# Kernel optimization log

Measured on AMD Instinct MI355X. Metric: run time of the kernel, lower is better.

The kernel has to match this reference:

```python
import math
import jax, jax.numpy as jnp
import numpy as np

B, S = 2, 2048
D, H, DK = 1024, 16, 64
M = 16            # nb_features
L = 4             # n_layers
DFF = 4096
VS, VT = 69, 69   # src/tgt vocab
NU = 10000        # num_users
FD = 34           # feature_dim
EPS = 1e-6


def make_pe(seq_len, d_model):
    pos = np.arange(seq_len, dtype=np.float32)[:, None]
    div = np.exp(np.arange(0, d_model, 2, dtype=np.float32) * (-math.log(10000.0) / d_model))
    pe = np.zeros((seq_len, d_model), np.float32)
    pe[:, 0::2] = np.sin(pos * div)
    pe[:, 1::2] = np.cos(pos * div)
    return jnp.asarray(pe)


def gelu_approx(x):
    return 0.5 * x * (1.0 + jnp.tanh(math.sqrt(2.0 / math.pi) * (x + 0.044715 * x ** 3)))


def layer_norm(x, alpha, bias):
    # torch LayerNormalization: unbiased std, eps added to std
    mu = x.mean(-1, keepdims=True)
    var = ((x - mu) ** 2).sum(-1, keepdims=True) / (x.shape[-1] - 1)
    return alpha * (x - mu) / (jnp.sqrt(var) + EPS) + bias


def setup_inputs():
    key = jax.random.key(0)
    ks = jax.random.split(key, 24)
    w = lambda k, shape, s=0.02: (jax.random.normal(k, shape, jnp.float32) * s)
    inp = {}
    inp['ids'] = jax.random.randint(ks[0], (B, S), 0, VS)
    inp['user_ids'] = jax.random.randint(ks[1], (B,), 0, NU)
    inp['id_embed'] = w(ks[2], (VS, D), 1.0)
    inp['feat_proj'] = w(ks[3], (D, FD))
    inp['gamma'] = jnp.float32(1.0)
    inp['gate_logits'] = w(ks[4], (NU, H))
    inp['wq'] = w(ks[5], (L, D, D))
    inp['wk'] = w(ks[6], (L, D, D))
    inp['wv'] = w(ks[7], (L, D, D))
    inp['wo'] = w(ks[8], (L, D, D))
    inp['omega'] = jax.random.normal(ks[9], (L, M, DK), jnp.float32) / math.sqrt(DK)
    inp['ln1_a'] = jnp.ones((L, D)); inp['ln1_b'] = jnp.zeros((L, D))
    inp['ln2_a'] = jnp.ones((L, D)); inp['ln2_b'] = jnp.zeros((L, D))
    inp['ff_w1'] = w(ks[10], (L, DFF, D)); inp['ff_b1'] = jnp.zeros((L, DFF))
    inp['ff_w2'] = w(ks[11], (L, D, DFF)); inp['ff_b2'] = jnp.zeros((L, D))
    inp['fin_a'] = jnp.ones((D,)); inp['fin_b'] = jnp.zeros((D,))
    inp['proj_w'] = w(ks[12], (VT, D)); inp['proj_b'] = jnp.zeros((VT,))
    inp['feat_tbl'] = w(ks[13], (VS, FD), 1.0)
    pm = np.zeros(VS, bool); pm[10:] = True   # ids >= 10 are products
    inp['prod_mask'] = jnp.asarray(pm)
    inp['pe'] = make_pe(S, D)
    return inp


def performer(xn, wq, wk, wv, wo, omega, gate):
    b, sq, _ = xn.shape
    q = (xn @ wq.T).reshape(b, sq, H, DK)
    k = (xn @ wk.T).reshape(b, sq, H, DK)
    v = (xn @ wv.T).reshape(b, sq, H, DK)
    # exp kernel feature map + row normalization
    qp = jnp.exp(-0.5 * (q @ omega.T) ** 2)        # (B,S,H,M)
    kp = jnp.exp(-0.5 * (k @ omega.T) ** 2)
    qp = qp / (qp.sum(-1, keepdims=True) + EPS)
    kp = kp / (kp.sum(-1, keepdims=True) + EPS)
    K_cum = jnp.cumsum(kp, axis=1)                              # (B,S,H,M)
    KV_cum = jnp.cumsum(kp[..., None] * v[..., None, :], axis=1)  # (B,S,H,M,DK)
    # blockwise causal index (block_size_h = block_size_w = 1)
    bh, bw = 1, 1
    ki = jnp.minimum((jnp.arange(sq) // bh + 1) * bw - 1, sq - 1)
    Ks = jnp.take(K_cum, ki, axis=1)
    KVs = jnp.take(KV_cum, ki, axis=1)
    num = jnp.einsum('bshm,bshmd->bshd', qp, KVs)
    den = jnp.sum(qp * Ks, -1, keepdims=True)
    out = num / (den + EPS)
    out = out * gate[:, None, :, None]
    return out.reshape(b, sq, D) @ wo.T


def reference(ids, user_ids, id_embed, feat_proj, gamma, gate_logits,
              wq, wk, wv, wo, omega, ln1_a, ln1_b, ln2_a, ln2_b,
              ff_w1, ff_b1, ff_w2, ff_b2, fin_a, fin_b,
              proj_w, proj_b, feat_tbl, prod_mask, pe):
    # SpecialPlusFeatureLookup
    id_vec = id_embed[ids]                       # (B,S,D)
    feat_vec = feat_tbl[ids] @ feat_proj.T       # (B,S,D)
    keep = prod_mask[ids]
    x = id_vec + gamma * (feat_vec * keep[..., None])
    # positional encoding (dropout=eval -> identity)
    x = x + pe[None, :x.shape[1], :]
    # per-user head gate
    gate = jax.nn.softmax(gate_logits[user_ids], axis=-1)  # (B,H)
    for l in range(L):
        x = x + performer(layer_norm(x, ln1_a[l], ln1_b[l]),
                          wq[l], wk[l], wv[l], wo[l], omega[l], gate)
        xn = layer_norm(x, ln2_a[l], ln2_b[l])
        x = x + (gelu_approx(xn @ ff_w1[l].T + ff_b1[l]) @ ff_w2[l].T + ff_b2[l])
    x = layer_norm(x, fin_a, fin_b)
    return x @ proj_w.T + proj_b                 # (B,S,VT)
```

## Files before the change

kernel.cpp:

```cpp
#include <hip/hip_runtime.h>
#include <hip/hip_bf16.h>
#include <math.h>

constexpr int BB  = 2;
constexpr int SS  = 2048;
constexpr int DD  = 1024;
constexpr int HH  = 16;
constexpr int DKK = 64;
constexpr int MB  = 16;
constexpr int LL  = 4;
constexpr int DF  = 4096;
constexpr int VSZ = 69;
constexpr int VTT = 69;
constexpr int FDD = 34;
constexpr float EPSF = 1e-6f;
constexpr int CL = 32;
constexpr int NC = SS / CL;

typedef unsigned short u16;
typedef unsigned int   u32;
using bf16x8 = __attribute__((ext_vector_type(8))) short;
using f32x4  = __attribute__((ext_vector_type(4))) float;

static __device__ __forceinline__ float b2f(u16 u) {
    union { u32 i; float f; } p; p.i = ((u32)u) << 16; return p.f;
}
static __device__ __forceinline__ u16 f2b(float f) {
    union { float f; u32 i; } p; p.f = f;
    u32 r = p.i + 0x7fffu + ((p.i >> 16) & 1u);
    return (u16)(r >> 16);
}
static __device__ __forceinline__ u32 pack2(float lo, float hi) {
    __hip_bfloat162 h = __float22bfloat162_rn(make_float2(lo, hi));
    return *(u32*)&h;
}
static __device__ __forceinline__ float gelu_f(float x) {
    float z = 0.7978845608028654f * (x + 0.044715f * x * x * x);
    z = fminf(fmaxf(z, -10.f), 10.f);
    float e = __expf(2.f * z);
    float th = (e - 1.f) / (e + 1.f);
    return 0.5f * x * (1.f + th);
}
static __device__ __forceinline__ float ldg1(const void* p, size_t i, int f32) {
    return f32 ? ((const float*)p)[i] : b2f(((const u16*)p)[i]);
}
static __device__ __forceinline__ float4 ldg4(const void* p, size_t i, int f32) {
    if (f32) return *(const float4*)((const float*)p + i);
    ushort4 u = *(const ushort4*)((const u16*)p + i);
    return make_float4(b2f(u.x), b2f(u.y), b2f(u.z), b2f(u.w));
}

#define GLD16(gp, lp) __builtin_amdgcn_global_load_lds( \
    (const __attribute__((address_space(1))) void*)(gp), \
    (__attribute__((address_space(3))) void*)(lp), 16, 0, 0)

__global__ void k_flag(const void* __restrict__ gamma, int* __restrict__ flag) {
    if (threadIdx.x == 0) *flag = (((const u16*)gamma)[0] == 0) ? 1 : 0;
}

__global__ __launch_bounds__(256) void k_build_tbl(
    const void* __restrict__ id_embed, const void* __restrict__ feat_tbl,
    const void* __restrict__ feat_proj, const void* __restrict__ gamma,
    const int* __restrict__ flagp, float* __restrict__ tbl)
{
    const int f32 = *flagp;
    int idx = blockIdx.x * 256 + threadIdx.x;
    if (idx >= VSZ * DD) return;
    int id = idx / DD, d = idx % DD;
    float acc = ldg1(id_embed, idx, f32);
    if (id >= 10) {
        float g = ldg1(gamma, 0, f32);
        float s = 0.f;
        for (int f = 0; f < FDD; ++f)
            s += ldg1(feat_tbl, (size_t)id * FDD + f, f32) * ldg1(feat_proj, (size_t)d * FDD + f, f32);
        acc += g * s;
    }
    tbl[idx] = acc;
}

__global__ __launch_bounds__(256) void k_gather(
    const float* __restrict__ tbl, const int* __restrict__ ids,
    const void* __restrict__ pe, const int* __restrict__ flagp, float* __restrict__ x)
{
    const int f32 = *flagp;
    int idx = blockIdx.x * 256 + threadIdx.x;
    int bs = idx >> 10, d = idx & (DD - 1);
    int s = bs & (SS - 1);
    x[idx] = tbl[ids[bs] * DD + d] + ldg1(pe, (size_t)s * DD + d, f32);
}

__global__ void k_gate(const void* __restrict__ gl, const int* __restrict__ uid,
                       const int* __restrict__ flagp, float* __restrict__ gate)
{
    const int f32 = *flagp;
    int b = threadIdx.x;
    if (b >= BB) return;
    size_t off = (size_t)uid[b] * HH;
    float v[HH], mx = -1e30f;
    for (int i = 0; i < HH; ++i) { v[i] = ldg1(gl, off + i, f32); mx = fmaxf(mx, v[i]); }
    float s = 0.f;
    for (int i = 0; i < HH; ++i) { v[i] = expf(v[i] - mx); s += v[i]; }
    for (int i = 0; i < HH; ++i) gate[b * HH + i] = v[i] / s;
}

__global__ __launch_bounds__(256) void k_layernorm(
    const float* __restrict__ x, const void* __restrict__ alpha,
    const void* __restrict__ beta, size_t p_off,
    const int* __restrict__ flagp, u16* __restrict__ y)
{
    const int f32 = *flagp;
    int row = blockIdx.x;
    const float* xr = x + (size_t)row * DD;
    int t = threadIdx.x;
    float v[4]; float s = 0.f;
    #pragma unroll
    for (int j = 0; j < 4; ++j) { v[j] = xr[t + j * 256]; s += v[j]; }
    __shared__ float red[8];
    int lane = t & 63, wv = t >> 6;
    #pragma unroll
    for (int off = 32; off > 0; off >>= 1) s += __shfl_down(s, off, 64);
    if (lane == 0) red[wv] = s;
    __syncthreads();
    float mu = (red[0] + red[1] + red[2] + red[3]) * (1.f / DD);
    __syncthreads();
    float ss = 0.f;
    #pragma unroll
    for (int j = 0; j < 4; ++j) { float dv = v[j] - mu; ss += dv * dv; }
    #pragma unroll
    for (int off = 32; off > 0; off >>= 1) ss += __shfl_down(ss, off, 64);
    if (lane == 0) red[wv] = ss;
    __syncthreads();
    float var = (red[0] + red[1] + red[2] + red[3]) * (1.f / (DD - 1));
    float rs = 1.f / (sqrtf(var) + EPSF);
    u16* yr = y + (size_t)row * DD;
    #pragma unroll
    for (int j = 0; j < 4; ++j) {
        int d = t + j * 256;
        yr[d] = f2b(ldg1(alpha, p_off + d, f32) * (v[j] - mu) * rs + ldg1(beta, p_off + d, f32));
    }
}

template<int BN, int BK>
static __device__ __forceinline__ void gemm_core(
    const u16* __restrict__ A, int lda,
    const void* __restrict__ W, size_t w_off, int ldw,
    const void* __restrict__ bias, size_t b_off, int f32,
    int K, int O, int act, int mode, u16* __restrict__ Cb, float* __restrict__ resid,
    int bx, int by)
{
    constexpr int NP  = BK / 32;
    constexpr int NI  = (BN == 128) ? 4 : 2;
    constexpr int WCOLS = (BN == 128) ? 4 : 2;
    __shared__ u16 As[NP * 64 * 32];
    __shared__ u16 Bs[NP * BN * 32];
    int t = threadIdx.x;
    int lane = t & 63, w = t >> 6;
    int quad = lane >> 4, l16 = lane & 15;
    int wm = (w / WCOLS) * (NI * 16);
    int wn = (w % WCOLS) * 32;
    int n0 = by * 64, o0 = bx * BN;

    f32x4 acc[NI][2];
    #pragma unroll
    for (int i = 0; i < NI; ++i)
        #pragma unroll
        for (int j = 0; j < 2; ++j)
            #pragma unroll
            for (int r = 0; r < 4; ++r) acc[i][j][r] = 0.f;

    int r0 = t >> 2;
    int swzt = (t >> 3) & 3;
    int c0  = (t & 3) * 8;
    int c0s = ((t & 3) ^ swzt) * 8;
    int tsw = ((t & ~3) | ((t & 3) ^ swzt));
    int quadx = quad ^ ((l16 >> 1) & 3);
    const u16* Ap = A + (size_t)n0 * lda + c0s;
    char* AsB = (char*)As;
    char* BsB = (char*)Bs;

    for (int k0 = 0; k0 < K; k0 += BK) {
        #pragma unroll
        for (int p = 0; p < NP; ++p) {
            int kk = k0 + p * 32;
            char* AsP = AsB + p * 4096;
            char* BsP = BsB + p * (BN * 64);
            GLD16(Ap + (size_t)r0 * lda + kk, AsP + t * 16);
            if (f32) {
                const float* Wf = (const float*)W + w_off + kk + c0;
                const float* q0 = Wf + (size_t)(o0 + r0) * ldw;
                float4 xa = *(const float4*)q0, xb = *(const float4*)(q0 + 4);
                uint4 pk;
                pk.x = pack2(xa.x, xa.y); pk.y = pack2(xa.z, xa.w);
                pk.z = pack2(xb.x, xb.y); pk.w = pack2(xb.z, xb.w);
                *(uint4*)(BsP + tsw * 16) = pk;
                if (BN == 128) {
                    const float* q1 = q0 + (size_t)64 * ldw;
                    float4 ya = *(const float4*)q1, yb = *(const float4*)(q1 + 4);
                    pk.x = pack2(ya.x, ya.y); pk.y = pack2(ya.z, ya.w);
                    pk.z = pack2(yb.x, yb.y); pk.w = pack2(yb.z, yb.w);
                    *(uint4*)(BsP + 4096 + tsw * 16) = pk;
                }
            } else {
                const u16* Wb = (const u16*)W + w_off + kk + c0s;
                GLD16(Wb + (size_t)(o0 + r0) * ldw, BsP + t * 16);
                if (BN == 128)
                    GLD16(Wb + (size_t)(o0 + r0 + 64) * ldw, BsP + 4096 + t * 16);
            }
        }
        __syncthreads();
        #pragma unroll
        for (int p = 0; p < NP; ++p) {
            const u16* AsP = As + p * (64 * 32);
            const u16* BsP = Bs + p * (BN * 32);
            bf16x8 af[NI], bfv[2];
            #pragma unroll
            for (int i = 0; i < NI; ++i)
                af[i] = *(const bf16x8*)(AsP + (size_t)(wm + i * 16 + l16) * 32 + quadx * 8);
            #pragma unroll
            for (int j = 0; j < 2; ++j)
                bfv[j] = *(const bf16x8*)(BsP + (size_t)(wn + j * 16 + l16) * 32 + quadx * 8);
            #pragma unroll
            for (int i = 0; i < NI; ++i)
                #pragma unroll
                for (int j = 0; j < 2; ++j)
                    acc[i][j] = __builtin_amdgcn_mfma_f32_16x16x32_bf16(af[i], bfv[j], acc[i][j], 0, 0, 0);
        }
        __syncthreads();
    }
    #pragma unroll
    for (int i = 0; i < NI; ++i) {
        #pragma unroll
        for (int j = 0; j < 2; ++j) {
            int col = o0 + wn + j * 16 + l16;
            float bval = bias ? ldg1(bias, b_off + col, f32) : 0.f;
            #pragma unroll
            for (int r = 0; r < 4; ++r) {
                int row = n0 + wm + i * 16 + quad * 4 + r;
                float val = acc[i][j][r] + bval;
                if (act) val = gelu_f(val);
                size_t idx = (size_t)row * O + col;
                if (mode == 1)      resid[idx] += val;
                else if (mode == 2) atomicAdd(&resid[idx], val);
                else                Cb[idx] = f2b(val);
            }
        }
    }
}

static __device__ __forceinline__ void xcd_tile(int& bx, int& by) {
    int gx = gridDim.x;
    int nwg = gx * gridDim.y;
    int h = blockIdx.y * gx + blockIdx.x;
    int q = nwg >> 3;
    int lid = (h & 7) * q + (h >> 3);
    bx = lid % gx; by = lid / gx;
}

__global__ __launch_bounds__(256, 8) void k_gemm_a(
    const u16* __restrict__ A, int lda, const void* __restrict__ W, size_t w_off, int ldw,
    const void* __restrict__ bias, size_t b_off, const int* __restrict__ flagp,
    int K, int O, int act, int mode, u16* __restrict__ Cb, float* __restrict__ resid)
{
    int bx, by; xcd_tile(bx, by);
    gemm_core<128, 32>(A, lda, W, w_off, ldw, bias, b_off, *flagp, K, O, act, mode, Cb, resid,
                       bx, by);
}

__global__ __launch_bounds__(256, 8) void k_gemm_b(
    const u16* __restrict__ A, int lda, const void* __restrict__ W, size_t w_off, int ldw,
    const void* __restrict__ bias, size_t b_off, const int* __restrict__ flagp,
    int K, int O, int act, int mode, u16* __restrict__ Cb, float* __restrict__ resid)
{
    int bx, by; xcd_tile(bx, by);
    gemm_core<64, 64>(A, lda, W, w_off, ldw, bias, b_off, *flagp, K, O, act, mode, Cb, resid,
                      bx, by);
}

__global__ __launch_bounds__(256) void k_gemm_qkv(
    const u16* __restrict__ A,
    const void* __restrict__ Wq, const void* __restrict__ Wk, const void* __restrict__ Wv,
    size_t w_off, const int* __restrict__ flagp,
    u16* __restrict__ oq, u16* __restrict__ ok, u16* __restrict__ ov)
{
    const void* W = (blockIdx.z == 0) ? Wq : (blockIdx.z == 1) ? Wk : Wv;
    u16* o = (blockIdx.z == 0) ? oq : (blockIdx.z == 1) ? ok : ov;
    int bx, by; xcd_tile(bx, by);
    gemm_core<128, 64>(A, DD, W, w_off, DD, nullptr, 0, *flagp, DD, DD, 0, 0, o, nullptr,
                       bx, by);
}

__global__ __launch_bounds__(256, 8) void k_gemm_wo(
    const u16* __restrict__ A, const void* __restrict__ W, size_t l_off_w,
    const int* __restrict__ flagp, float* __restrict__ resid)
{
    int c = blockIdx.z;
    int bx, by; xcd_tile(bx, by);
    gemm_core<64, 64>(A + (size_t)c * 512, DD, W, l_off_w + (size_t)c * 512, DD,
                      nullptr, 0, *flagp, 512, DD, 0, 2, nullptr, resid, bx, by);
}

__global__ __launch_bounds__(256, 8) void k_gemm_ff2(
    const u16* __restrict__ A, const void* __restrict__ W, size_t l_off_w,
    const void* __restrict__ bias, size_t l_off_b, const int* __restrict__ flagp,
    float* __restrict__ resid)
{
    int c = blockIdx.z;
    int bx, by; xcd_tile(bx, by);
    gemm_core<64, 64>(A + (size_t)c * 2048, DF, W, l_off_w + (size_t)c * 2048, DF,
                      (c == 0) ? bias : nullptr, l_off_b, *flagp,
                      2048, DD, 0, 2, nullptr, resid, bx, by);
}

__global__ __launch_bounds__(256) void k_gemm_small(
    const u16* __restrict__ A, const void* __restrict__ W, size_t w_off, int ldw,
    const void* __restrict__ bias, size_t b_off,
    const int* __restrict__ flagp, int K, int O, void* __restrict__ outp)
{
    const int f32 = *flagp;
    __shared__ float As[16][68];
    __shared__ float Ws[16][68];
    int t = threadIdx.x;
    int tx = t & 15, ty = t >> 4;
    int o0 = blockIdx.x * 64, n0 = blockIdx.y * 64;
    int lr = t >> 2;
    int lk = (t & 3) * 4;
    float c[4][4] = {};
    for (int k0 = 0; k0 < K; k0 += 16) {
        ushort4 av = *(const ushort4*)(A + (size_t)(n0 + lr) * K + k0 + lk);
        As[lk + 0][lr] = b2f(av.x); As[lk + 1][lr] = b2f(av.y);
        As[lk + 2][lr] = b2f(av.z); As[lk + 3][lr] = b2f(av.w);
        float4 wv4 = make_float4(0.f, 0.f, 0.f, 0.f);
        int orow = o0 + lr;
        if (orow < O) wv4 = ldg4(W, w_off + (size_t)orow * ldw + k0 + lk, f32);
        Ws[lk + 0][lr] = wv4.x; Ws[lk + 1][lr] = wv4.y;
        Ws[lk + 2][lr] = wv4.z; Ws[lk + 3][lr] = wv4.w;
        __syncthreads();
        #pragma unroll
        for (int kk = 0; kk < 16; ++kk) {
            float4 a = *(const float4*)&As[kk][ty * 4];
            float4 b = *(const float4*)&Ws[kk][tx * 4];
            c[0][0] += a.x * b.x; c[0][1] += a.x * b.y; c[0][2] += a.x * b.z; c[0][3] += a.x * b.w;
            c[1][0] += a.y * b.x; c[1][1] += a.y * b.y; c[1][2] += a.y * b.z; c[1][3] += a.y * b.w;
            c[2][0] += a.z * b.x; c[2][1] += a.z * b.y; c[2][2] += a.z * b.z; c[2][3] += a.z * b.w;
            c[3][0] += a.w * b.x; c[3][1] += a.w * b.y; c[3][2] += a.w * b.z; c[3][3] += a.w * b.w;
        }
        __syncthreads();
    }
    #pragma unroll
    for (int i = 0; i < 4; ++i) {
        int n = n0 + ty * 4 + i;
        #pragma unroll
        for (int j = 0; j < 4; ++j) {
            int o = o0 + tx * 4 + j;
            if (o >= O) continue;
            float val = c[i][j];
            if (bias) val += ldg1(bias, b_off + o, f32);
            size_t idx = (size_t)n * O + o;
            if (f32) ((float*)outp)[idx] = val;
            else     ((u16*)outp)[idx] = f2b(val);
        }
    }
}

__global__ __launch_bounds__(256) void k_featmap(
    const u16* __restrict__ q, const void* __restrict__ omega, size_t o_off,
    const int* __restrict__ flagp, u16* __restrict__ qp_t)
{
    const int f32 = *flagp;
    __shared__ float q_s[64][68];
    __shared__ float om_s[16][68];
    int t = threadIdx.x;
    int bh = blockIdx.y, b = bh >> 4, h = bh & 15;
    int s0 = blockIdx.x * 64;
    const u16* qbase = q + (size_t)(b * SS + s0) * DD + h * DKK;
    #pragma unroll
    for (int i = 0; i < 2; ++i) {
        int idx = i * 256 + t;
        int si = idx >> 3, part = idx & 7;
        uint4 raw = *(const uint4*)(qbase + (size_t)si * DD + part * 8);
        const u16* pr = (const u16*)&raw;
        *(float4*)&q_s[si][part * 8]     = make_float4(b2f(pr[0]), b2f(pr[1]), b2f(pr[2]), b2f(pr[3]));
        *(float4*)&q_s[si][part * 8 + 4] = make_float4(b2f(pr[4]), b2f(pr[5]), b2f(pr[6]), b2f(pr[7]));
    }
    #pragma unroll
    for (int i = 0; i < 4; ++i) {
        int idx = i * 256 + t;
        om_s[idx >> 6][idx & 63] = ldg1(omega, o_off + idx, f32);
    }
    __syncthreads();
    int s = t >> 2, mg = t & 3;
    float u[4] = {0.f, 0.f, 0.f, 0.f};
    #pragma unroll
    for (int dk = 0; dk < 64; dk += 4) {
        float4 q4 = *(const float4*)&q_s[s][dk];
        #pragma unroll
        for (int mj = 0; mj < 4; ++mj) {
            float4 o4 = *(const float4*)&om_s[mg * 4 + mj][dk];
            u[mj] += q4.x * o4.x + q4.y * o4.y + q4.z * o4.z + q4.w * o4.w;
        }
    }
    float phi[4], tot = 0.f;
    #pragma unroll
    for (int mj = 0; mj < 4; ++mj) { phi[mj] = expf(-0.5f * u[mj] * u[mj]); tot += phi[mj]; }
    tot += __shfl_xor(tot, 1); tot += __shfl_xor(tot, 2);
    float inv = 1.f / (tot + EPSF);
    uint2 out;
    out.x = pack2(phi[0] * inv, phi[1] * inv);
    out.y = pack2(phi[2] * inv, phi[3] * inv);
    *(uint2*)(qp_t + ((size_t)bh * SS + s0 + s) * MB + mg * 4) = out;
}

__global__ __launch_bounds__(64) void k_scan_part(
    const u16* __restrict__ kp_t, const u16* __restrict__ v,
    float* __restrict__ kv_tot, float* __restrict__ kc_tot)
{
    int c = blockIdx.x, bh = blockIdx.y;
    int b = bh >> 4, h = bh & 15;
    int d = threadIdx.x;
    __shared__ float kp_s[CL * MB];
    const u16* kpb = kp_t + ((size_t)bh * SS + c * CL) * MB;
    #pragma unroll
    for (int i = 0; i < CL * MB / 64; ++i) {
        int idx = i * 64 + d;
        kp_s[idx] = b2f(kpb[idx]);
    }
    __syncthreads();
    float Kc[MB], KV[MB];
    #pragma unroll
    for (int m = 0; m < MB; ++m) { Kc[m] = 0.f; KV[m] = 0.f; }
    const u16* vp = v + ((size_t)b * SS + c * CL) * DD + h * DKK + d;
    for (int si = 0; si < CL; ++si) {
        float vd = b2f(vp[(size_t)si * DD]);
        #pragma unroll
        for (int m = 0; m < MB; ++m) {
            float kp = kp_s[si * MB + m];
            Kc[m] += kp; KV[m] += kp * vd;
        }
    }
    float* kvp = kv_tot + (((size_t)bh * NC + c) * MB) * DKK + d;
    #pragma unroll
    for (int m = 0; m < MB; ++m) kvp[(size_t)m * DKK] = KV[m];
    #pragma unroll
    for (int m = 0; m < MB; ++m)
        if (d == m) kc_tot[((size_t)bh * NC + c) * MB + m] = Kc[m];
}

__global__ __launch_bounds__(64) void k_scan_off(
    float* __restrict__ kv_tot, float* __restrict__ kc_tot)
{
    int bh = blockIdx.x; int d = threadIdx.x;
    if (d < MB) {
        float run = 0.f;
        for (int c = 0; c < NC; ++c) {
            size_t i = ((size_t)bh * NC + c) * MB + d;
            float tt = kc_tot[i]; kc_tot[i] = run; run += tt;
        }
    }
    float run[MB];
    #pragma unroll
    for (int m = 0; m < MB; ++m) run[m] = 0.f;
    for (int c = 0; c < NC; ++c) {
        size_t base = (((size_t)bh * NC + c) * MB) * DKK + d;
        float tt[MB];
        #pragma unroll
        for (int m = 0; m < MB; ++m) tt[m] = kv_tot[base + (size_t)m * DKK];
        #pragma unroll
        for (int m = 0; m < MB; ++m) { kv_tot[base + (size_t)m * DKK] = run[m]; run[m] += tt[m]; }
    }
}

__global__ __launch_bounds__(64) void k_scan_out(
    const u16* __restrict__ qp_t, const u16* __restrict__ kp_t, const u16* __restrict__ v,
    const float* __restrict__ kv_tot, const float* __restrict__ kc_tot,
    const float* __restrict__ gate, u16* __restrict__ attn)
{
    int c = blockIdx.x, bh = blockIdx.y;
    int b = bh >> 4, h = bh & 15;
    int d = threadIdx.x;
    __shared__ float kp_s[CL * MB], qp_s[CL * MB];
    const u16* kpb = kp_t + ((size_t)bh * SS + c * CL) * MB;
    const u16* qpb = qp_t + ((size_t)bh * SS + c * CL) * MB;
    #pragma unroll
    for (int i = 0; i < CL * MB / 64; ++i) {
        int idx = i * 64 + d;
        kp_s[idx] = b2f(kpb[idx]);
        qp_s[idx] = b2f(qpb[idx]);
    }
    __syncthreads();
    float Kc[MB], KV[MB];
    const float* kvp = kv_tot + (((size_t)bh * NC + c) * MB) * DKK + d;
    const float* kcp = kc_tot + ((size_t)bh * NC + c) * MB;
    #pragma unroll
    for (int m = 0; m < MB; ++m) { KV[m] = kvp[(size_t)m * DKK]; Kc[m] = kcp[m]; }
    float g = gate[bh];
    const u16* vp = v + ((size_t)b * SS + c * CL) * DD + h * DKK + d;
    u16* ap = attn + ((size_t)b * SS + c * CL) * DD + h * DKK + d;
    for (int si = 0; si < CL; ++si) {
        float vd = b2f(vp[(size_t)si * DD]);
        float num = 0.f, den = 0.f;
        #pragma unroll
        for (int m = 0; m < MB; ++m) {
            float kp = kp_s[si * MB + m];
            Kc[m] += kp; KV[m] += kp * vd;
            float qp = qp_s[si * MB + m];
            num += qp * KV[m]; den += qp * Kc[m];
        }
        ap[(size_t)si * DD] = f2b(num / (den + EPSF) * g);
    }
}

extern "C" void kernel_launch(void* const* d_in, const int* in_sizes, int n_in,
                              void* d_out, int out_size, void* d_ws, size_t ws_size,
                              hipStream_t stream)
{
    const int*  ids       = (const int*)d_in[0];
    const int*  user_ids  = (const int*)d_in[1];
    const void* id_embed  = d_in[2];
    const void* feat_proj = d_in[3];
    const void* gamma     = d_in[4];
    const void* gate_log  = d_in[5];
    const void* wq        = d_in[6];
    const void* wk        = d_in[7];
    const void* wv        = d_in[8];
    const void* wo        = d_in[9];
    const void* omega     = d_in[10];
    const void* ln1_a     = d_in[11];
    const void* ln1_b     = d_in[12];
    const void* ln2_a     = d_in[13];
    const void* ln2_b     = d_in[14];
    const void* ff_w1     = d_in[15];
    const void* ff_b1     = d_in[16];
    const void* ff_w2     = d_in[17];
    const void* ff_b2     = d_in[18];
    const void* fin_a     = d_in[19];
    const void* fin_b     = d_in[20];
    const void* proj_w    = d_in[21];
    const void* proj_b    = d_in[22];
    const void* feat_tbl  = d_in[23];
    const void* pe        = d_in[25];

    char* base = (char*)d_ws;
    const size_t MiB = (size_t)1 << 20;
    int*   flagp  = (int*)base;
    float* gate   = (float*)(base + 64);
    float* kc_tot = (float*)(base + 4096);
    float* tbl    = (float*)(base + 256 * 1024);
    float* x      = (float*)(base + 1 * MiB);
    u16*   xn     = (u16*)  (base + 17 * MiB);
    float* kv_tot = (float*)(base + 17 * MiB);
    u16*   qb     = (u16*)  (base + 25 * MiB);
    u16*   kb     = (u16*)  (base + 33 * MiB);
    u16*   vb     = (u16*)  (base + 41 * MiB);
    u16*   qp_t   = (u16*)  (base + 49 * MiB);
    u16*   kp_t   = (u16*)  (base + 51 * MiB);
    u16*   attn   = qb;
    u16*   ff1c   = qb;
    u16*   ff1f   = qb;
    const bool merged_ffn = (ws_size >= 57 * MiB);

    const int NT = BB * SS;

    k_flag<<<1, 64, 0, stream>>>(gamma, flagp);
    k_build_tbl<<<(VSZ * DD + 255) / 256, 256, 0, stream>>>(id_embed, feat_tbl, feat_proj, gamma, flagp, tbl);
    k_gather<<<(NT * DD) / 256, 256, 0, stream>>>(tbl, ids, pe, flagp, x);
    k_gate<<<1, 64, 0, stream>>>(gate_log, user_ids, flagp, gate);

    dim3 gQKV(DD / 128, NT / 64, 3);
    dim3 gWo(DD / 64, NT / 64, 2);
    dim3 gF1m(DF / 128, NT / 64);
    dim3 gF2m(DD / 64, NT / 64, 2);
    dim3 gF1(2048 / 128, NT / 64);
    dim3 gF2(DD / 64, NT / 64);
    dim3 gFeat(SS / 64, BB * HH);
    dim3 gScan(NC, BB * HH);

    for (int l = 0; l < LL; ++l) {
        size_t lDD = (size_t)l * DD * DD;
        k_layernorm<<<NT, 256, 0, stream>>>(x, ln1_a, ln1_b, (size_t)l * DD, flagp, xn);
        k_gemm_qkv<<<gQKV, 256, 0, stream>>>(xn, wq, wk, wv, lDD, flagp, qb, kb, vb);
        k_featmap<<<gFeat, 256, 0, stream>>>(qb, omega, (size_t)l * MB * DKK, flagp, qp_t);
        k_featmap<<<gFeat, 256, 0, stream>>>(kb, omega, (size_t)l * MB * DKK, flagp, kp_t);
        k_scan_part<<<gScan, 64, 0, stream>>>(kp_t, vb, kv_tot, kc_tot);
        k_scan_off<<<BB * HH, 64, 0, stream>>>(kv_tot, kc_tot);
        k_scan_out<<<gScan, 64, 0, stream>>>(qp_t, kp_t, vb, kv_tot, kc_tot, gate, attn);
        k_gemm_wo<<<gWo, 256, 0, stream>>>(attn, wo, lDD, flagp, x);
        k_layernorm<<<NT, 256, 0, stream>>>(x, ln2_a, ln2_b, (size_t)l * DD, flagp, xn);
        if (merged_ffn) {
            k_gemm_a<<<gF1m, 256, 0, stream>>>(xn, DD, ff_w1, (size_t)l * DF * DD, DD,
                                               ff_b1, (size_t)l * DF, flagp,
                                               DD, DF, 1, 0, ff1f, nullptr);
            k_gemm_ff2<<<gF2m, 256, 0, stream>>>(ff1f, ff_w2, (size_t)l * DD * DF, ff_b2,
                                                 (size_t)l * DD, flagp, x);
        } else {
            for (int c = 0; c < 2; ++c) {
                size_t w1_off = (size_t)l * DF * DD + (size_t)c * 2048 * DD;
                size_t b1_off = (size_t)l * DF + c * 2048;
                size_t w2_off = (size_t)l * DD * DF + (size_t)c * 2048;
                k_gemm_a<<<gF1, 256, 0, stream>>>(xn, DD, ff_w1, w1_off, DD, ff_b1, b1_off, flagp, DD, 2048, 1, 0, ff1c, nullptr);
                k_gemm_b<<<gF2, 256, 0, stream>>>(ff1c, 2048, ff_w2, w2_off, DF,
                                                  (c == 0) ? ff_b2 : nullptr, (size_t)l * DD,
                                                  flagp, 2048, DD, 0, 1, nullptr, x);
            }
        }
    }
    k_layernorm<<<NT, 256, 0, stream>>>(x, fin_a, fin_b, 0, flagp, xn);
    dim3 g4((VTT + 63) / 64, NT / 64);
    k_gemm_small<<<g4, 256, 0, stream>>>(xn, proj_w, 0, DD, proj_b, 0, flagp, DD, VTT, d_out);
}
```

Measured before the change: 1.790 ms.

## Switch all GEMMs to a 128x128 block tile with 64x64 warp tiles

Replaces the parameterized 64xBN GEMM core with a single 128x128 tile (BK=64), where each of four warps computes a 64x64 subtile with a 4x4 grid of MFMAs. This raises arithmetic intensity per shared-memory load and halves global reloads of A and W. The Wo and FF2 split-K factor grows from 2 to 4, giving more atomic adds but keeping enough blocks. The cost is higher register and LDS use per block, so occupancy drops (launch bounds lowered to 4).

New measurement: 1.691 ms. 1.06x faster.

```diff
diff --git a/kernel.cpp b/kernel.cpp
--- a/kernel.cpp
+++ b/kernel.cpp
@@ -140,31 +140,29 @@
     }
 }
 
-template<int BN, int BK>
-static __device__ __forceinline__ void gemm_core(
+template<int BK>
+static __device__ __forceinline__ void gemm_core128(
     const u16* __restrict__ A, int lda,
     const void* __restrict__ W, size_t w_off, int ldw,
     const void* __restrict__ bias, size_t b_off, int f32,
     int K, int O, int act, int mode, u16* __restrict__ Cb, float* __restrict__ resid,
     int bx, int by)
 {
-    constexpr int NP  = BK / 32;
-    constexpr int NI  = (BN == 128) ? 4 : 2;
-    constexpr int WCOLS = (BN == 128) ? 4 : 2;
-    __shared__ u16 As[NP * 64 * 32];
-    __shared__ u16 Bs[NP * BN * 32];
+    constexpr int NP = BK / 32;
+    __shared__ u16 As[NP * 128 * 32];
+    __shared__ u16 Bs[NP * 128 * 32];
     int t = threadIdx.x;
     int lane = t & 63, w = t >> 6;
     int quad = lane >> 4, l16 = lane & 15;
-    int wm = (w / WCOLS) * (NI * 16);
-    int wn = (w % WCOLS) * 32;
-    int n0 = by * 64, o0 = bx * BN;
-
-    f32x4 acc[NI][2];
-    #pragma unroll
-    for (int i = 0; i < NI; ++i)
-        #pragma unroll
-        for (int j = 0; j < 2; ++j)
+    int wm = (w >> 1) * 64;
+    int wn = (w & 1) * 64;
+    int n0 = by * 128, o0 = bx * 128;
+
+    f32x4 acc[4][4];
+    #pragma unroll
+    for (int i = 0; i < 4; ++i)
+        #pragma unroll
+        for (int j = 0; j < 4; ++j)
             #pragma unroll
             for (int r = 0; r < 4; ++r) acc[i][j][r] = 0.f;
 
@@ -182,55 +180,53 @@
         #pragma unroll
         for (int p = 0; p < NP; ++p) {
             int kk = k0 + p * 32;
-            char* AsP = AsB + p * 4096;
-            char* BsP = BsB + p * (BN * 64);
+            char* AsP = AsB + p * 8192;
+            char* BsP = BsB + p * 8192;
             GLD16(Ap + (size_t)r0 * lda + kk, AsP + t * 16);
+            GLD16(Ap + (size_t)(r0 + 64) * lda + kk, AsP + 4096 + t * 16);
             if (f32) {
                 const float* Wf = (const float*)W + w_off + kk + c0;
                 const float* q0 = Wf + (size_t)(o0 + r0) * ldw;
+                const float* q1 = q0 + (size_t)64 * ldw;
                 float4 xa = *(const float4*)q0, xb = *(const float4*)(q0 + 4);
                 uint4 pk;
                 pk.x = pack2(xa.x, xa.y); pk.y = pack2(xa.z, xa.w);
                 pk.z = pack2(xb.x, xb.y); pk.w = pack2(xb.z, xb.w);
                 *(uint4*)(BsP + tsw * 16) = pk;
-                if (BN == 128) {
-                    const float* q1 = q0 + (size_t)64 * ldw;
-                    float4 ya = *(const float4*)q1, yb = *(const float4*)(q1 + 4);
-                    pk.x = pack2(ya.x, ya.y); pk.y = pack2(ya.z, ya.w);
-                    pk.z = pack2(yb.x, yb.y); pk.w = pack2(yb.z, yb.w);
-                    *(uint4*)(BsP + 4096 + tsw * 16) = pk;
-                }
+                float4 ya = *(const float4*)q1, yb = *(const float4*)(q1 + 4);
+                pk.x = pack2(ya.x, ya.y); pk.y = pack2(ya.z, ya.w);
+                pk.z = pack2(yb.x, yb.y); pk.w = pack2(yb.z, yb.w);
+                *(uint4*)(BsP + 4096 + tsw * 16) = pk;
             } else {
                 const u16* Wb = (const u16*)W + w_off + kk + c0s;
                 GLD16(Wb + (size_t)(o0 + r0) * ldw, BsP + t * 16);
-                if (BN == 128)
-                    GLD16(Wb + (size_t)(o0 + r0 + 64) * ldw, BsP + 4096 + t * 16);
+                GLD16(Wb + (size_t)(o0 + r0 + 64) * ldw, BsP + 4096 + t * 16);
             }
         }
         __syncthreads();
         #pragma unroll
         for (int p = 0; p < NP; ++p) {
-            const u16* AsP = As + p * (64 * 32);
-            const u16* BsP = Bs + p * (BN * 32);
-            bf16x8 af[NI], bfv[2];
+            const u16* AsP = As + p * (128 * 32);
+            const u16* BsP = Bs + p * (128 * 32);
+            bf16x8 af[4], bfv[4];
             #pragma unroll
-            for (int i = 0; i < NI; ++i)
+            for (int i = 0; i < 4; ++i)
                 af[i] = *(const bf16x8*)(AsP + (size_t)(wm + i * 16 + l16) * 32 + quadx * 8);
             #pragma unroll
-            for (int j = 0; j < 2; ++j)
+            for (int j = 0; j < 4; ++j)
                 bfv[j] = *(const bf16x8*)(BsP + (size_t)(wn + j * 16 + l16) * 32 + quadx * 8);
             #pragma unroll
-            for (int i = 0; i < NI; ++i)
+            for (int i = 0; i < 4; ++i)
                 #pragma unroll
-                for (int j = 0; j < 2; ++j)
+                for (int j = 0; j < 4; ++j)
                     acc[i][j] = __builtin_amdgcn_mfma_f32_16x16x32_bf16(af[i], bfv[j], acc[i][j], 0, 0, 0);
         }
         __syncthreads();
     }
     #pragma unroll
-    for (int i = 0; i < NI; ++i) {
-        #pragma unroll
-        for (int j = 0; j < 2; ++j) {
+    for (int i = 0; i < 4; ++i) {
+        #pragma unroll
+        for (int j = 0; j < 4; ++j) {
             int col = o0 + wn + j * 16 + l16;
             float bval = bias ? ldg1(bias, b_off + col, f32) : 0.f;
             #pragma unroll
@@ -256,27 +252,17 @@
     bx = lid % gx; by = lid / gx;
 }
 
-__global__ __launch_bounds__(256, 8) void k_gemm_a(
+__global__ __launch_bounds__(256, 4) void k_gemm_a(
     const u16* __restrict__ A, int lda, const void* __restrict__ W, size_t w_off, int ldw,
     const void* __restrict__ bias, size_t b_off, const int* __restrict__ flagp,
     int K, int O, int act, int mode, u16* __restrict__ Cb, float* __restrict__ resid)
 {
     int bx, by; xcd_tile(bx, by);
-    gemm_core<128, 32>(A, lda, W, w_off, ldw, bias, b_off, *flagp, K, O, act, mode, Cb, resid,
-                       bx, by);
-}
-
-__global__ __launch_bounds__(256, 8) void k_gemm_b(
-    const u16* __restrict__ A, int lda, const void* __restrict__ W, size_t w_off, int ldw,
-    const void* __restrict__ bias, size_t b_off, const int* __restrict__ flagp,
-    int K, int O, int act, int mode, u16* __restrict__ Cb, float* __restrict__ resid)
-{
-    int bx, by; xcd_tile(bx, by);
-    gemm_core<64, 64>(A, lda, W, w_off, ldw, bias, b_off, *flagp, K, O, act, mode, Cb, resid,
-                      bx, by);
-}
-
-__global__ __launch_bounds__(256) void k_gemm_qkv(
+    gemm_core128<64>(A, lda, W, w_off, ldw, bias, b_off, *flagp, K, O, act, mode, Cb, resid,
+                     bx, by);
+}
+
+__global__ __launch_bounds__(256, 4) void k_gemm_qkv(
     const u16* __restrict__ A,
     const void* __restrict__ Wq, const void* __restrict__ Wk, const void* __restrict__ Wv,
     size_t w_off, const int* __restrict__ flagp,
@@ -285,30 +271,30 @@
     const void* W = (blockIdx.z == 0) ? Wq : (blockIdx.z == 1) ? Wk : Wv;
     u16* o = (blockIdx.z == 0) ? oq : (blockIdx.z == 1) ? ok : ov;
     int bx, by; xcd_tile(bx, by);
-    gemm_core<128, 64>(A, DD, W, w_off, DD, nullptr, 0, *flagp, DD, DD, 0, 0, o, nullptr,
-                       bx, by);
-}
-
-__global__ __launch_bounds__(256, 8) void k_gemm_wo(
+    gemm_core128<64>(A, DD, W, w_off, DD, nullptr, 0, *flagp, DD, DD, 0, 0, o, nullptr,
+                     bx, by);
+}
+
+__global__ __launch_bounds__(256, 4) void k_gemm_wo(
     const u16* __restrict__ A, const void* __restrict__ W, size_t l_off_w,
     const int* __restrict__ flagp, float* __restrict__ resid)
 {
     int c = blockIdx.z;
     int bx, by; xcd_tile(bx, by);
-    gemm_core<64, 64>(A + (size_t)c * 512, DD, W, l_off_w + (size_t)c * 512, DD,
-                      nullptr, 0, *flagp, 512, DD, 0, 2, nullptr, resid, bx, by);
-}
-
-__global__ __launch_bounds__(256, 8) void k_gemm_ff2(
+    gemm_core128<64>(A + (size_t)c * 256, DD, W, l_off_w + (size_t)c * 256, DD,
+                     nullptr, 0, *flagp, 256, DD, 0, 2, nullptr, resid, bx, by);
+}
+
+__global__ __launch_bounds__(256, 4) void k_gemm_ff2(
     const u16* __restrict__ A, const void* __restrict__ W, size_t l_off_w,
     const void* __restrict__ bias, size_t l_off_b, const int* __restrict__ flagp,
     float* __restrict__ resid)
 {
     int c = blockIdx.z;
     int bx, by; xcd_tile(bx, by);
-    gemm_core<64, 64>(A + (size_t)c * 2048, DF, W, l_off_w + (size_t)c * 2048, DF,
-                      (c == 0) ? bias : nullptr, l_off_b, *flagp,
-                      2048, DD, 0, 2, nullptr, resid, bx, by);
+    gemm_core128<64>(A + (size_t)c * 1024, DF, W, l_off_w + (size_t)c * 1024, DF,
+                     (c == 0) ? bias : nullptr, l_off_b, *flagp,
+                     1024, DD, 0, 2, nullptr, resid, bx, by);
 }
 
 __global__ __launch_bounds__(256) void k_gemm_small(
@@ -565,12 +551,12 @@
     k_gather<<<(NT * DD) / 256, 256, 0, stream>>>(tbl, ids, pe, flagp, x);
     k_gate<<<1, 64, 0, stream>>>(gate_log, user_ids, flagp, gate);
 
-    dim3 gQKV(DD / 128, NT / 64, 3);
-    dim3 gWo(DD / 64, NT / 64, 2);
-    dim3 gF1m(DF / 128, NT / 64);
-    dim3 gF2m(DD / 64, NT / 64, 2);
-    dim3 gF1(2048 / 128, NT / 64);
-    dim3 gF2(DD / 64, NT / 64);
+    dim3 gQKV(DD / 128, NT / 128, 3);
+    dim3 gWo(DD / 128, NT / 128, 4);
+    dim3 gF1m(DF / 128, NT / 128);
+    dim3 gF2m(DD / 128, NT / 128, 4);
+    dim3 gF1(2048 / 128, NT / 128);
+    dim3 gF2(DD / 128, NT / 128);
     dim3 gFeat(SS / 64, BB * HH);
     dim3 gScan(NC, BB * HH);
 
@@ -597,7 +583,7 @@
                 size_t b1_off = (size_t)l * DF + c * 2048;
                 size_t w2_off = (size_t)l * DD * DF + (size_t)c * 2048;
                 k_gemm_a<<<gF1, 256, 0, stream>>>(xn, DD, ff_w1, w1_off, DD, ff_b1, b1_off, flagp, DD, 2048, 1, 0, ff1c, nullptr);
-                k_gemm_b<<<gF2, 256, 0, stream>>>(ff1c, 2048, ff_w2, w2_off, DF,
+                k_gemm_a<<<gF2, 256, 0, stream>>>(ff1c, 2048, ff_w2, w2_off, DF,
                                                   (c == 0) ? ff_b2 : nullptr, (size_t)l * DD,
                                                   flagp, 2048, DD, 0, 1, nullptr, x);
             }
```
